# Optimization experiments

Hardware: AMD Instinct MI355X
Metric: run time of the kernel (lower is better)

Reference implementation:

```python
import jax, jax.numpy as jnp
import numpy as np

NUM_USERS = 100000
NUM_MOVIES = 50000
NUM_EDGES = 4000000
USER_FEAT = 24
MOVIE_FEAT = 404
HID = 64
GENRES = 3


def setup_inputs() -> dict:
    key = jax.random.key(0)
    ks = jax.random.split(key, 16)
    inp = {
        'x_user': jax.random.normal(ks[0], (NUM_USERS, USER_FEAT), jnp.float32),
        'x_movie': jax.random.normal(ks[1], (NUM_MOVIES, MOVIE_FEAT), jnp.float32),
        'edge_src': jax.random.randint(ks[2], (NUM_EDGES,), 0, NUM_USERS, jnp.int32),
        'edge_dst': jax.random.randint(ks[3], (NUM_EDGES,), 0, NUM_MOVIES, jnp.int32),
        'W_user': jax.random.normal(ks[4], (HID, USER_FEAT), jnp.float32) * 0.1,
        'b_user': jax.random.normal(ks[5], (HID,), jnp.float32) * 0.1,
        'W_movie': jax.random.normal(ks[6], (HID, MOVIE_FEAT), jnp.float32) * 0.05,
        'b_movie': jax.random.normal(ks[7], (HID,), jnp.float32) * 0.1,
        'Wl1_um': jax.random.normal(ks[8], (HID, HID), jnp.float32) * 0.1,
        'bl1_um': jax.random.normal(ks[9], (HID,), jnp.float32) * 0.1,
        'Wr1_um': jax.random.normal(ks[10], (HID, HID), jnp.float32) * 0.1,
        'Wl1_mu': jax.random.normal(ks[11], (HID, HID), jnp.float32) * 0.1,
        'bl1_mu': jax.random.normal(ks[12], (HID,), jnp.float32) * 0.1,
        'Wr1_mu': jax.random.normal(ks[13], (HID, HID), jnp.float32) * 0.1,
        'Wl2_um': jax.random.normal(ks[14], (GENRES, HID), jnp.float32) * 0.1,
        'bl2_um': jnp.zeros((GENRES,), jnp.float32),
        'Wr2_um': jax.random.normal(ks[15], (GENRES, HID), jnp.float32) * 0.1,
    }
    return inp


def _mean_agg(src_x, src_idx, dst_idx, num_dst):
    # gather messages [E, C], scatter-sum to dst, divide by degree (mean aggr)
    msg = src_x[src_idx]
    s = jax.ops.segment_sum(msg, dst_idx, num_segments=num_dst)
    cnt = jax.ops.segment_sum(jnp.ones_like(dst_idx, jnp.float32), dst_idx, num_segments=num_dst)
    return s / jnp.maximum(cnt, 1.0)[:, None]


def _sage(agg, x_dst, Wl, bl, Wr):
    # SAGEConv: lin_l(mean_aggr(x_j)) + lin_r(x_dst); bias only on lin_l
    return agg @ Wl.T + bl + x_dst @ Wr.T


def reference(x_user, x_movie, edge_src, edge_dst, W_user, b_user, W_movie, b_movie,
              Wl1_um, bl1_um, Wr1_um, Wl1_mu, bl1_mu, Wr1_mu, Wl2_um, bl2_um, Wr2_um):
    nu, nm = x_user.shape[0], x_movie.shape[0]
    # input projections
    hu = x_user @ W_user.T + b_user    # [U, H]
    hm = x_movie @ W_movie.T + b_movie  # [M, H]
    # layer 1 (hetero: one SAGEConv per edge type; undirected -> both directions)
    m1 = _sage(_mean_agg(hu, edge_src, edge_dst, nm), hm, Wl1_um, bl1_um, Wr1_um)
    u1 = _sage(_mean_agg(hm, edge_dst, edge_src, nu), hu, Wl1_mu, bl1_mu, Wr1_mu)
    m1 = jax.nn.relu(m1)
    u1 = jax.nn.relu(u1)
    # dropout is identity in eval mode
    # layer 2: only movie output is returned
    out = _sage(_mean_agg(u1, edge_src, edge_dst, nm), m1, Wl2_um, bl2_um, Wr2_um)
    return out
```

## Files before the change

kernel.cpp:

```cpp
#include <hip/hip_runtime.h>


constexpr int NU = 100000;
constexpr int NM = 50000;
constexpr int NE = 4000000;
constexpr int FU = 24;
constexpr int FM = 404;
constexpr int HD = 64;

constexpr int BSH = 8;
constexpr int MBK = (NM + 255) >> BSH;
constexpr int UBK = (NU + 255) >> BSH;
constexpr int NBK = MBK + UBK;
constexpr int EPB = 8192;
constexpr int CAPE = 28672;

static inline size_t alignup(size_t x) { return (x + 255) & ~size_t(255); }

__device__ __forceinline__ float bf2f(unsigned short h) {
  return __uint_as_float(((unsigned int)h) << 16);
}
__device__ __forceinline__ unsigned short f2bf(float f) {
  unsigned int u = __float_as_uint(f);
  u = (u + 0x7FFFu + ((u >> 16) & 1u)) >> 16;
  return (unsigned short)u;
}
__device__ __forceinline__ float2 unpk(unsigned u) {
  return make_float2(__uint_as_float(u << 16), __uint_as_float(u & 0xFFFF0000u));
}
__device__ __forceinline__ float fp8dec(unsigned v) {
  unsigned u = ((v & 0x80u) << 24) | ((v & 0x7Fu) << 20);
  return __uint_as_float(u) * 0x1p120f;
}
__device__ __forceinline__ unsigned char f2fp8(float f) {
  float a = fminf(fabsf(f), 448.0f);
  unsigned u = __float_as_uint(a * 0x1p-120f);
  u = u + 0x7FFFFu + ((u >> 20) & 1u);
  return (unsigned char)(((u >> 20) & 0x7Fu) | ((__float_as_uint(f) >> 24) & 0x80u));
}

typedef __attribute__((ext_vector_type(2))) float f2v;

#if __has_builtin(__builtin_amdgcn_cvt_pk_f32_fp8)
#define FP8_HW 1
#endif

__device__ __forceinline__ f2v fp8lo(unsigned w) {
#ifdef FP8_HW
  return __builtin_amdgcn_cvt_pk_f32_fp8(w, false);
#else
  f2v r; r.x = fp8dec(w); r.y = fp8dec(w >> 8); return r;
#endif
}
__device__ __forceinline__ f2v fp8hi(unsigned w) {
#ifdef FP8_HW
  return __builtin_amdgcn_cvt_pk_f32_fp8(w, true);
#else
  f2v r; r.x = fp8dec(w >> 16); r.y = fp8dec(w >> 24); return r;
#endif
}
__device__ __forceinline__ unsigned pk2bf(float x, float y) {
  return (unsigned)f2bf(x) | ((unsigned)f2bf(y) << 16);
}

using bf16x8 = __attribute__((ext_vector_type(8))) short;
using f32x4  = __attribute__((ext_vector_type(4))) float;


__global__ __launch_bounds__(256) void histB_kernel(const int* __restrict__ src,
                                                    const int* __restrict__ dst,
                                                    int* __restrict__ bh) {
  __shared__ int h[NBK];
  for (int i = threadIdx.x; i < NBK; i += 256) h[i] = 0;
  __syncthreads();
  int idx = blockIdx.x * 256 + threadIdx.x;
  int stride = gridDim.x * 256;
  for (int i = idx; i < NE; i += stride) {
    atomicAdd(&h[dst[i] >> BSH], 1);
    atomicAdd(&h[MBK + (src[i] >> BSH)], 1);
  }
  __syncthreads();
  for (int i = threadIdx.x; i < NBK; i += 256) {
    int c = h[i];
    if (c) atomicAdd(&bh[i], c);
  }
}

__global__ __launch_bounds__(1024) void scanB_kernel(const int* __restrict__ bh,
                                                     int* __restrict__ bbase_m,
                                                     int* __restrict__ bbase_u,
                                                     int* __restrict__ bcur_m,
                                                     int* __restrict__ bcur_u) {
  __shared__ int tmp[1024];
  int t = threadIdx.x;
  int vm = (t < MBK) ? bh[t] : 0;
  tmp[t] = vm;
  __syncthreads();
  for (int off = 1; off < 1024; off <<= 1) {
    int v = (t >= off) ? tmp[t - off] : 0;
    __syncthreads();
    tmp[t] += v;
    __syncthreads();
  }
  if (t < MBK) {
    int e = tmp[t] - vm;
    bbase_m[t] = e; bcur_m[t] = e;
    if (t == MBK - 1) bbase_m[MBK] = tmp[t];
  }
  __syncthreads();
  int vu = (t < UBK) ? bh[MBK + t] : 0;
  tmp[t] = vu;
  __syncthreads();
  for (int off = 1; off < 1024; off <<= 1) {
    int v = (t >= off) ? tmp[t - off] : 0;
    __syncthreads();
    tmp[t] += v;
    __syncthreads();
  }
  if (t < UBK) {
    int e = tmp[t] - vu;
    bbase_u[t] = e; bcur_u[t] = e;
    if (t == UBK - 1) bbase_u[UBK] = tmp[t];
  }
}

__global__ __launch_bounds__(1024) void passA_kernel(
    const int* __restrict__ src, const int* __restrict__ dst,
    int* __restrict__ bcur_m, int* __restrict__ bcur_u,
    unsigned* __restrict__ stage_m, unsigned* __restrict__ stage_u) {
  __shared__ int hB[NBK];
  __shared__ int cntB[NBK];
  __shared__ int gB[NBK];
  __shared__ int tmp[1024];
  __shared__ unsigned binM[EPB];
  __shared__ unsigned binU[EPB];
  int t = threadIdx.x;
  for (int i = t; i < NBK; i += 1024) hB[i] = 0;
  __syncthreads();
  int e0 = blockIdx.x * EPB + t;
  int sv[8], dv[8], rm[8], ru[8];
#pragma unroll
  for (int k = 0; k < 8; ++k) {
    int e = e0 + k * 1024;
    if (e < NE) {
      int s = src[e], d = dst[e];
      sv[k] = s; dv[k] = d;
      rm[k] = atomicAdd(&hB[d >> BSH], 1);
      ru[k] = atomicAdd(&hB[MBK + (s >> BSH)], 1);
    } else {
      sv[k] = -1;
    }
  }
  __syncthreads();
  int cm = (t < MBK) ? hB[t] : 0;
  tmp[t] = cm;
  __syncthreads();
  for (int off = 1; off < 1024; off <<= 1) {
    int v = (t >= off) ? tmp[t - off] : 0;
    __syncthreads();
    tmp[t] += v;
    __syncthreads();
  }
  int lofsM = tmp[t] - cm;
  __syncthreads();
  int cu_ = (t < UBK) ? hB[MBK + t] : 0;
  tmp[t] = cu_;
  __syncthreads();
  for (int off = 1; off < 1024; off <<= 1) {
    int v = (t >= off) ? tmp[t - off] : 0;
    __syncthreads();
    tmp[t] += v;
    __syncthreads();
  }
  int lofsU = tmp[t] - cu_;
  __syncthreads();
  if (t < MBK) { cntB[t] = cm; hB[t] = lofsM; }
  if (t < UBK) { cntB[MBK + t] = cu_; hB[MBK + t] = lofsU; }
  __syncthreads();
#pragma unroll
  for (int k = 0; k < 8; ++k) {
    if (sv[k] >= 0) {
      int s = sv[k], d = dv[k];
      binM[hB[d >> BSH] + rm[k]] = ((unsigned)(d & 255) << 24) | (unsigned)s;
      binU[hB[MBK + (s >> BSH)] + ru[k]] = ((unsigned)(s & 255) << 24) | (unsigned)d;
    }
  }
  __syncthreads();
  for (int b = t; b < NBK; b += 1024) {
    int cc = cntB[b];
    if (cc) {
      int gb = (b < MBK) ? atomicAdd(&bcur_m[b], cc) : atomicAdd(&bcur_u[b - MBK], cc);
      gB[b] = gb - hB[b];
    }
  }
  __syncthreads();
  int wv = t >> 6, ln = t & 63;
  for (int b = wv; b < MBK; b += 16) {
    int cc = cntB[b], lo = hB[b], go = hB[b] + gB[b];
    for (int j = ln; j < cc; j += 64) stage_m[go + j] = binM[lo + j];
  }
  for (int b = wv; b < UBK; b += 16) {
    int cc = cntB[MBK + b], lo = hB[MBK + b], go = hB[MBK + b] + gB[MBK + b];
    for (int j = ln; j < cc; j += 64) stage_u[go + j] = binU[lo + j];
  }
}

__global__ __launch_bounds__(1024) void passB_kernel(
    const int* __restrict__ bbase_m, const int* __restrict__ bbase_u,
    const unsigned* __restrict__ stage_m, const unsigned* __restrict__ stage_u,
    int* __restrict__ csr_m, int* __restrict__ csr_u,
    int* __restrict__ rp_m, int* __restrict__ rp_u) {
  __shared__ int cnt[256];
  __shared__ int sc[256];
  extern __shared__ unsigned sbuf[];
  int b = blockIdx.x;
  const unsigned* stage; int* csr; int* rp; int idbase, ntot, bb, be;
  if (b < MBK) {
    stage = stage_m; csr = csr_m; rp = rp_m;
    idbase = b << BSH; ntot = NM;
    bb = bbase_m[b]; be = bbase_m[b + 1];
  } else {
    int c = b - MBK;
    stage = stage_u; csr = csr_u; rp = rp_u;
    idbase = c << BSH; ntot = NU;
    bb = bbase_u[c]; be = bbase_u[c + 1];
  }
  int nloc = min(256, ntot - idbase);
  int t = threadIdx.x;
  int span = be - bb;
  if (t < 256) cnt[t] = 0;
  __syncthreads();
  for (int j = bb + t; j < be; j += 1024) atomicAdd(&cnt[stage[j] >> 24], 1);
  __syncthreads();
  int c0 = (t < 256) ? cnt[t] : 0;
  if (t < 256) sc[t] = c0;
  __syncthreads();
  for (int off = 1; off < 256; off <<= 1) {
    int v = 0;
    if (t < 256 && t >= off) v = sc[t - off];
    __syncthreads();
    if (t < 256) sc[t] += v;
    __syncthreads();
  }
  if (t < nloc) {
    rp[idbase + t] = bb + sc[t] - c0;
    cnt[t] = sc[t] - c0;
  }
  if (t == 0 && idbase + nloc == ntot) rp[ntot] = be;
  __syncthreads();
  if (span <= CAPE) {
    for (int j = bb + t; j < be; j += 1024) {
      unsigned e = stage[j];
      int pos = atomicAdd(&cnt[e >> 24], 1);
      sbuf[pos] = e & 0xFFFFFFu;
    }
    __syncthreads();
    for (int j = t; j < span; j += 1024) csr[bb + j] = (int)sbuf[j];
  } else {
    for (int j = bb + t; j < be; j += 1024) {
      unsigned e = stage[j];
      int pos = atomicAdd(&cnt[e >> 24], 1);
      csr[bb + pos] = (int)(e & 0xFFFFFFu);
    }
  }
}


__global__ void convXu_kernel(const float* __restrict__ xu, unsigned char* __restrict__ xu8) {
  int i = blockIdx.x * 256 + threadIdx.x;
  if (i < NU * 32) {
    int r = i >> 5, c = i & 31;
    xu8[i] = (c < FU) ? f2fp8(xu[r * FU + c]) : 0;
  }
}

__global__ void convXu16_kernel(const float* __restrict__ xu, unsigned short* __restrict__ xb) {
  int i = blockIdx.x * 256 + threadIdx.x;
  if (i < NU * 32) {
    int r = i >> 5, c = i & 31;
    unsigned short v = 0;
    if (c < FU) v = f2bf(xu[r * FU + c]);
    else if (c == 31) v = 0x3F80;
    xb[i] = v;
  }
}

__global__ void convW_kernel(const float* __restrict__ W, unsigned short* __restrict__ Wb,
                             int n) {
  int i = blockIdx.x * 256 + threadIdx.x;
  if (i < n) Wb[i] = f2bf(W[i]);
}

__global__ void convWum_kernel(const float* __restrict__ Wl, const float* __restrict__ Wu,
                               const float* __restrict__ bu, const float* __restrict__ Wr,
                               unsigned short* __restrict__ W96) {
  int i = blockIdx.x * 256 + threadIdx.x;
  if (i >= 64 * 96) return;
  int h = i / 96, k = i - h * 96;
  float v = 0.f;
  if (k < FU) {
    for (int j = 0; j < 64; ++j) v += Wl[h * 64 + j] * Wu[j * FU + k];
  } else if (k == 31) {
    for (int j = 0; j < 64; ++j) v += Wl[h * 64 + j] * bu[j];
  } else if (k >= 32) {
    v = Wr[h * 64 + (k - 32)];
  }
  W96[i] = f2bf(v);
}

__global__ void convWmu_kernel(const float* __restrict__ Wl, const float* __restrict__ Wr,
                               const float* __restrict__ Wu, const float* __restrict__ bu,
                               unsigned short* __restrict__ W96) {
  int i = blockIdx.x * 256 + threadIdx.x;
  if (i >= 64 * 96) return;
  int h = i / 96, k = i - h * 96;
  float v = 0.f;
  if (k < 64) {
    v = Wl[h * 64 + k];
  } else if (k < 64 + FU) {
    for (int j = 0; j < 64; ++j) v += Wr[h * 64 + j] * Wu[j * FU + (k - 64)];
  } else if (k == 95) {
    for (int j = 0; j < 64; ++j) v += Wr[h * 64 + j] * bu[j];
  }
  W96[i] = f2bf(v);
}

__global__ __launch_bounds__(256) void proj_movie_kernel(
    const float* __restrict__ xm, const unsigned short* __restrict__ Wb,
    const float* __restrict__ bm, unsigned short* __restrict__ hm,
    unsigned char* __restrict__ hm8) {
  __shared__ unsigned short Xs[64][72];
  __shared__ unsigned short Ws[64][72];
  int t = threadIdx.x;
  int lane = t & 63, wid = t >> 6;
  int row0 = blockIdx.x * 64;
  int r0 = wid * 16;
  f32x4 acc[4];
#pragma unroll
  for (int nt = 0; nt < 4; ++nt) acc[nt] = (f32x4){0.f, 0.f, 0.f, 0.f};

  for (int k0 = 0; k0 < 448; k0 += 64) {
    int kc = min(64, FM - k0);
    __syncthreads();
    for (int i = t; i < 1024; i += 256) {
      int r = i >> 4, c4 = i & 15;
      float4 v = make_float4(0.f, 0.f, 0.f, 0.f);
      if (c4 * 4 < kc && row0 + r < NM)
        v = *(const float4*)(xm + (size_t)(row0 + r) * FM + k0 + c4 * 4);
      ushort4 o;
      o.x = f2bf(v.x); o.y = f2bf(v.y); o.z = f2bf(v.z); o.w = f2bf(v.w);
      *(ushort4*)&Xs[r][c4 * 4] = o;
    }
    for (int i = t; i < 1024; i += 256) {
      int h = i >> 4, c4 = i & 15;
      uint2 v = make_uint2(0u, 0u);
      if (c4 * 4 < kc)
        v = *(const uint2*)(Wb + (size_t)h * FM + k0 + c4 * 4);
      *(uint2*)&Ws[h][c4 * 4] = v;
    }
    __syncthreads();
#pragma unroll
    for (int kk = 0; kk < 64; kk += 32) {
      bf16x8 a = *(const bf16x8*)&Xs[r0 + (lane & 15)][kk + (lane >> 4) * 8];
#pragma unroll
      for (int nt = 0; nt < 4; ++nt) {
        bf16x8 b = *(const bf16x8*)&Ws[nt * 16 + (lane & 15)][kk + (lane >> 4) * 8];
        acc[nt] = __builtin_amdgcn_mfma_f32_16x16x32_bf16(a, b, acc[nt], 0, 0, 0);
      }
    }
  }
  int col = lane & 15;
  int rbase = r0 + (lane >> 4) * 4;
#pragma unroll
  for (int nt = 0; nt < 4; ++nt) {
    float b = bm[nt * 16 + col];
#pragma unroll
    for (int j = 0; j < 4; ++j) {
      int row = row0 + rbase + j;
      if (row < NM) {
        float v = acc[nt][j] + b;
        hm[(size_t)row * HD + nt * 16 + col] = f2bf(v);
        hm8[(size_t)row * HD + nt * 16 + col] = f2fp8(v);
      }
    }
  }
}


__global__ __launch_bounds__(256) void agg24z_kernel(
    const unsigned char* __restrict__ xu8, const int* __restrict__ rp,
    const int* __restrict__ csr, unsigned short* __restrict__ a24,
    float* __restrict__ zagg, int n) {
  int wid = threadIdx.x >> 6, lane = threadIdx.x & 63;
  int g = lane >> 3, fq = lane & 7;
  int row = blockIdx.x * 32 + wid * 8 + g;
  if (row >= n) return;
  int beg = rp[row], end = rp[row + 1];
  const unsigned char* tb = xu8 + fq * 4;
  f2v a01 = {0.f, 0.f}, a23 = {0.f, 0.f};
  int i = beg;
  for (; i + 4 <= end; i += 4) {
    unsigned o0 = (unsigned)csr[i] << 5;
    unsigned o1 = (unsigned)csr[i + 1] << 5;
    unsigned o2 = (unsigned)csr[i + 2] << 5;
    unsigned o3 = (unsigned)csr[i + 3] << 5;
    unsigned w0 = *(const unsigned*)(tb + o0);
    unsigned w1 = *(const unsigned*)(tb + o1);
    unsigned w2 = *(const unsigned*)(tb + o2);
    unsigned w3 = *(const unsigned*)(tb + o3);
    a01 += (fp8lo(w0) + fp8lo(w1)) + (fp8lo(w2) + fp8lo(w3));
    a23 += (fp8hi(w0) + fp8hi(w1)) + (fp8hi(w2) + fp8hi(w3));
  }
  for (; i < end; ++i) {
    unsigned w = *(const unsigned*)(tb + ((unsigned)csr[i] << 5));
    a01 += fp8lo(w);
    a23 += fp8hi(w);
  }
  float inv = 1.0f / fmaxf((float)(end - beg), 1.0f);
  uint2 o;
  o.x = pk2bf(a01.x * inv, a01.y * inv);
  o.y = pk2bf(a23.x * inv, a23.y * inv);
  if (fq == 7)
    o.y = (o.y & 0xFFFFu) | ((end > beg ? 0x3F80u : 0u) << 16);
  if (fq == 6)
    *(float4*)(zagg + (size_t)row * 4) =
        make_float4(a01.x * inv, a01.y * inv, a23.x * inv, 0.f);
  *(uint2*)(a24 + (size_t)row * 32 + fq * 4) = o;
}


__global__ __launch_bounds__(256) void aggU_kernel(
    const unsigned char* __restrict__ tab8, const int* __restrict__ rp,
    const int* __restrict__ csr, unsigned short* __restrict__ out, int n) {
  int wid = threadIdx.x >> 6, lane = threadIdx.x & 63;
  int g = lane >> 3, fq = lane & 7;
  int row = blockIdx.x * 32 + wid * 8 + g;
  if (row >= n) return;
  int beg = rp[row], end = rp[row + 1];
  const unsigned char* tb = tab8 + fq * 8;
  f2v a01 = {0.f, 0.f}, a23 = {0.f, 0.f}, a45 = {0.f, 0.f}, a67 = {0.f, 0.f};
  int i = beg;
  for (; i + 4 <= end; i += 4) {
    unsigned o0 = (unsigned)csr[i] << 6;
    unsigned o1 = (unsigned)csr[i + 1] << 6;
    unsigned o2 = (unsigned)csr[i + 2] << 6;
    unsigned o3 = (unsigned)csr[i + 3] << 6;
    uint2 w0 = *(const uint2*)(tb + o0);
    uint2 w1 = *(const uint2*)(tb + o1);
    uint2 w2 = *(const uint2*)(tb + o2);
    uint2 w3 = *(const uint2*)(tb + o3);
    a01 += (fp8lo(w0.x) + fp8lo(w1.x)) + (fp8lo(w2.x) + fp8lo(w3.x));
    a23 += (fp8hi(w0.x) + fp8hi(w1.x)) + (fp8hi(w2.x) + fp8hi(w3.x));
    a45 += (fp8lo(w0.y) + fp8lo(w1.y)) + (fp8lo(w2.y) + fp8lo(w3.y));
    a67 += (fp8hi(w0.y) + fp8hi(w1.y)) + (fp8hi(w2.y) + fp8hi(w3.y));
  }
  for (; i < end; ++i) {
    uint2 w = *(const uint2*)(tb + ((unsigned)csr[i] << 6));
    a01 += fp8lo(w.x); a23 += fp8hi(w.x);
    a45 += fp8lo(w.y); a67 += fp8hi(w.y);
  }
  float inv = 1.0f / fmaxf((float)(end - beg), 1.0f);
  uint4 o;
  o.x = pk2bf(a01.x * inv, a01.y * inv);
  o.y = pk2bf(a23.x * inv, a23.y * inv);
  o.z = pk2bf(a45.x * inv, a45.y * inv);
  o.w = pk2bf(a67.x * inv, a67.y * inv);
  *(uint4*)(out + (size_t)row * HD + fq * 8) = o;
}


__global__ __launch_bounds__(256) void sage_um_kernel(
    const unsigned short* __restrict__ a24, const unsigned short* __restrict__ hm,
    const unsigned short* __restrict__ W96, const float* __restrict__ bl,
    unsigned short* __restrict__ m1, int n) {
  __shared__ unsigned short Xs[64][104];
  __shared__ unsigned short Ws[64][104];
  int t = threadIdx.x;
  int lane = t & 63, wid = t >> 6;
  int row0 = blockIdx.x * 64;
  int r0 = wid * 16;
  for (int i = t; i < 768; i += 256) {
    int h = i / 12, g = i - h * 12;
    *(uint4*)&Ws[h][g * 8] = *(const uint4*)(W96 + (size_t)h * 96 + g * 8);
  }
  for (int i = t; i < 768; i += 256) {
    int r = i / 12, g = i - r * 12;
    uint4 v = make_uint4(0u, 0u, 0u, 0u);
    if (row0 + r < n) {
      if (g < 4) v = *(const uint4*)(a24 + (size_t)(row0 + r) * 32 + g * 8);
      else       v = *(const uint4*)(hm + (size_t)(row0 + r) * HD + (g - 4) * 8);
    }
    *(uint4*)&Xs[r][g * 8] = v;
  }
  __syncthreads();
  f32x4 acc[4];
#pragma unroll
  for (int nt = 0; nt < 4; ++nt) acc[nt] = (f32x4){0.f, 0.f, 0.f, 0.f};
#pragma unroll
  for (int kk = 0; kk < 96; kk += 32) {
    bf16x8 a = *(const bf16x8*)&Xs[r0 + (lane & 15)][kk + (lane >> 4) * 8];
#pragma unroll
    for (int nt = 0; nt < 4; ++nt) {
      bf16x8 b = *(const bf16x8*)&Ws[nt * 16 + (lane & 15)][kk + (lane >> 4) * 8];
      acc[nt] = __builtin_amdgcn_mfma_f32_16x16x32_bf16(a, b, acc[nt], 0, 0, 0);
    }
  }
  int col = lane & 15;
  int rbase = r0 + (lane >> 4) * 4;
#pragma unroll
  for (int nt = 0; nt < 4; ++nt) {
    float b = bl[nt * 16 + col];
#pragma unroll
    for (int j = 0; j < 4; ++j) {
      int row = row0 + rbase + j;
      if (row < n)
        m1[(size_t)row * HD + nt * 16 + col] = f2bf(fmaxf(acc[nt][j] + b, 0.f));
    }
  }
}


__global__ __launch_bounds__(256) void sage96u_kernel(
    const unsigned short* __restrict__ agg, const unsigned short* __restrict__ xb,
    const unsigned short* __restrict__ W96, const float* __restrict__ bl,
    unsigned short* __restrict__ u1, int n) {
  __shared__ unsigned short Xs[64][104];
  __shared__ unsigned short Ws[64][104];
  int t = threadIdx.x;
  int lane = t & 63, wid = t >> 6;
  int row0 = blockIdx.x * 64;
  int r0 = wid * 16;
  for (int i = t; i < 768; i += 256) {
    int h = i / 12, g = i - h * 12;
    *(uint4*)&Ws[h][g * 8] = *(const uint4*)(W96 + (size_t)h * 96 + g * 8);
  }
  for (int i = t; i < 768; i += 256) {
    int r = i / 12, g = i - r * 12;
    uint4 v = make_uint4(0u, 0u, 0u, 0u);
    if (row0 + r < n) {
      if (g < 8) v = *(const uint4*)(agg + (size_t)(row0 + r) * HD + g * 8);
      else       v = *(const uint4*)(xb + (size_t)(row0 + r) * 32 + (g - 8) * 8);
    }
    *(uint4*)&Xs[r][g * 8] = v;
  }
  __syncthreads();
  f32x4 acc[4];
#pragma unroll
  for (int nt = 0; nt < 4; ++nt) acc[nt] = (f32x4){0.f, 0.f, 0.f, 0.f};
#pragma unroll
  for (int kk = 0; kk < 96; kk += 32) {
    bf16x8 a = *(const bf16x8*)&Xs[r0 + (lane & 15)][kk + (lane >> 4) * 8];
#pragma unroll
    for (int nt = 0; nt < 4; ++nt) {
      bf16x8 b = *(const bf16x8*)&Ws[nt * 16 + (lane & 15)][kk + (lane >> 4) * 8];
      acc[nt] = __builtin_amdgcn_mfma_f32_16x16x32_bf16(a, b, acc[nt], 0, 0, 0);
    }
  }
  int col = lane & 15;
  int rbase = r0 + (lane >> 4) * 4;
#pragma unroll
  for (int nt = 0; nt < 4; ++nt) {
    float b = bl[nt * 16 + col];
#pragma unroll
    for (int j = 0; j < 4; ++j) {
      int row = row0 + rbase + j;
      if (row < n)
        u1[(size_t)row * HD + nt * 16 + col] = f2bf(fmaxf(acc[nt][j] + b, 0.f));
    }
  }
}


__global__ __launch_bounds__(256) void zproj_kernel(
    const unsigned short* __restrict__ u1, const float* __restrict__ Wl2,
    unsigned char* __restrict__ xu8) {
  __shared__ float W[3][64];
  int t = threadIdx.x;
  if (t < 192) W[t / 64][t & 63] = Wl2[t];
  __syncthreads();
  int wid = t >> 6, lane = t & 63;
  int g = lane >> 4, fq = lane & 15;
  int row = blockIdx.x * 16 + wid * 4 + g;
  if (row >= NU) return;
  uint2 v = *(const uint2*)(u1 + (size_t)row * HD + fq * 4);
  float2 p0 = unpk(v.x), p1 = unpk(v.y);
  int f = fq * 4;
  float z0 = p0.x * W[0][f] + p0.y * W[0][f + 1] + p1.x * W[0][f + 2] + p1.y * W[0][f + 3];
  float z1 = p0.x * W[1][f] + p0.y * W[1][f + 1] + p1.x * W[1][f + 2] + p1.y * W[1][f + 3];
  float z2 = p0.x * W[2][f] + p0.y * W[2][f + 1] + p1.x * W[2][f + 2] + p1.y * W[2][f + 3];
#pragma unroll
  for (int off = 1; off < 16; off <<= 1) {
    z0 += __shfl_xor(z0, off);
    z1 += __shfl_xor(z1, off);
    z2 += __shfl_xor(z2, off);
  }
  if (fq == 0) {
    unsigned w = (unsigned)f2fp8(z0) | ((unsigned)f2fp8(z1) << 8)
               | ((unsigned)f2fp8(z2) << 16);
    *(unsigned*)(xu8 + (size_t)row * 32 + 24) = w;
  }
}

__global__ void out2_kernel(const float* __restrict__ zagg,
                            const unsigned short* __restrict__ m1,
                            const float* __restrict__ Wr2, const float* __restrict__ bl2,
                            float* __restrict__ out, int n) {
  int wid = threadIdx.x >> 6, lane = threadIdx.x & 63;
  int row = blockIdx.x * 4 + wid;
  if (row >= n) return;
  float mm = bf2f(m1[(size_t)row * HD + lane]);
#pragma unroll
  for (int g = 0; g < 3; ++g) {
    float p = mm * Wr2[g * HD + lane];
#pragma unroll
    for (int off = 32; off > 0; off >>= 1) p += __shfl_down(p, off);
    if (lane == 0) out[row * 3 + g] = p + zagg[row * 4 + g] + bl2[g];
  }
}


extern "C" void kernel_launch(void* const* d_in, const int* in_sizes, int n_in,
                              void* d_out, int out_size, void* d_ws, size_t ws_size,
                              hipStream_t stream) {
  const float* x_user  = (const float*)d_in[0];
  const float* x_movie = (const float*)d_in[1];
  const int*   e_src   = (const int*)d_in[2];
  const int*   e_dst   = (const int*)d_in[3];
  const float* W_user  = (const float*)d_in[4];
  const float* b_user  = (const float*)d_in[5];
  const float* W_movie = (const float*)d_in[6];
  const float* b_movie = (const float*)d_in[7];
  const float* Wl1_um  = (const float*)d_in[8];
  const float* bl1_um  = (const float*)d_in[9];
  const float* Wr1_um  = (const float*)d_in[10];
  const float* Wl1_mu  = (const float*)d_in[11];
  const float* bl1_mu  = (const float*)d_in[12];
  const float* Wr1_mu  = (const float*)d_in[13];
  const float* Wl2_um  = (const float*)d_in[14];
  const float* bl2_um  = (const float*)d_in[15];
  const float* Wr2_um  = (const float*)d_in[16];
  float* outp = (float*)d_out;

  char* p = (char*)d_ws;
  size_t off = 0;
  auto take = [&](size_t bytes) { void* r = p + off; off += alignup(bytes); return r; };

  int* rp_m    = (int*)take(size_t(NM + 1) * 4);
  int* rp_u    = (int*)take(size_t(NU + 1) * 4);
  int* bh      = (int*)take(size_t(NBK) * 4);
  int* bbase_m = (int*)take(size_t(MBK + 1) * 4);
  int* bbase_u = (int*)take(size_t(UBK + 1) * 4);
  int* bcur_m  = (int*)take(size_t(MBK) * 4);
  int* bcur_u  = (int*)take(size_t(UBK) * 4);
  int* csr_m   = (int*)take(size_t(NE) * 4);
  int* csr_u   = (int*)take(size_t(NE) * 4);

  size_t ov_base = off;
  unsigned* stage_m = (unsigned*)take(size_t(NE) * 4);
  unsigned* stage_u = (unsigned*)take(size_t(NE) * 4);
  size_t stage_end = off;
  off = ov_base;
  unsigned short* hm    = (unsigned short*)take(size_t(NM) * HD * 2);
  unsigned short* u1    = (unsigned short*)take(size_t(NU) * HD * 2);
  unsigned short* m1    = (unsigned short*)take(size_t(NM) * HD * 2);
  unsigned short* aggb  = (unsigned short*)take(size_t(NU) * HD * 2);
  unsigned char*  xu8   = (unsigned char*)take(size_t(NU) * 32);
  unsigned char*  hm8   = (unsigned char*)take(size_t(NM) * HD);
  unsigned short* a24   = (unsigned short*)take(size_t(NM) * 32 * 2);
  unsigned short* xub16 = (unsigned short*)take(size_t(NU) * 32 * 2);
  if (off < stage_end) off = stage_end;
  float* zagg = (float*)take(size_t(NM) * 16);
  unsigned short* Wb    = (unsigned short*)take(size_t(HD) * FM * 2);
  unsigned short* Wum96 = (unsigned short*)take(size_t(HD) * 96 * 2);
  unsigned short* Wmu96 = (unsigned short*)take(size_t(HD) * 96 * 2);
  if (off > ws_size) return;

  const int TB = 256;

  hipMemsetAsync(bh, 0, size_t(NBK) * 4, stream);
  histB_kernel<<<512, 256, 0, stream>>>(e_src, e_dst, bh);
  scanB_kernel<<<1, 1024, 0, stream>>>(bh, bbase_m, bbase_u, bcur_m, bcur_u);
  passA_kernel<<<(NE + EPB - 1) / EPB, 1024, 0, stream>>>(e_src, e_dst, bcur_m, bcur_u,
                                                          stage_m, stage_u);
  passB_kernel<<<NBK, 1024, CAPE * 4, stream>>>(bbase_m, bbase_u, stage_m, stage_u,
                                                csr_m, csr_u, rp_m, rp_u);

  convW_kernel<<<(HD * FM + 255) / 256, 256, 0, stream>>>(W_movie, Wb, HD * FM);
  convWum_kernel<<<(64 * 96 + 255) / 256, 256, 0, stream>>>(Wl1_um, W_user, b_user,
                                                            Wr1_um, Wum96);
  convWmu_kernel<<<(64 * 96 + 255) / 256, 256, 0, stream>>>(Wl1_mu, Wr1_mu, W_user,
                                                            b_user, Wmu96);
  convXu_kernel<<<(NU * 32 + 255) / 256, 256, 0, stream>>>(x_user, xu8);
  convXu16_kernel<<<(NU * 32 + 255) / 256, 256, 0, stream>>>(x_user, xub16);
  proj_movie_kernel<<<(NM + 63) / 64, TB, 0, stream>>>(x_movie, Wb, b_movie, hm, hm8);

  aggU_kernel<<<(NU + 31) / 32, TB, 0, stream>>>(hm8, rp_u, csr_u, aggb, NU);
  sage96u_kernel<<<(NU + 63) / 64, TB, 0, stream>>>(aggb, xub16, Wmu96, bl1_mu, u1, NU);
  zproj_kernel<<<(NU + 15) / 16, TB, 0, stream>>>(u1, Wl2_um, xu8);

  agg24z_kernel<<<(NM + 31) / 32, TB, 0, stream>>>(xu8, rp_m, csr_m, a24, zagg, NM);
  sage_um_kernel<<<(NM + 63) / 64, TB, 0, stream>>>(a24, hm, Wum96, bl1_um, m1, NM);

  out2_kernel<<<(NM + 3) / 4, TB, 0, stream>>>(zagg, m1, Wr2_um, bl2_um, outp, NM);
}
```

Before: 270.1 us.

## Preload padded movie weights to LDS and double-buffer X tiles in projection

The movie weight matrix is padded to 448 columns and loaded into shared memory once per block, instead of being re-staged each k-chunk. The x_movie tile is double-buffered: the next chunk's global loads are issued into registers before the MFMA work on the current chunk and written to the other LDS buffer afterwards, leaving one barrier per iteration. This aims to hide global-load latency in proj_movie, which streams about 80MB of fp32 input. In exchange, LDS use rises to about 77KB per block, which may lower occupancy, and more registers are held live.

```diff
diff --git a/kernel.cpp b/kernel.cpp
--- a/kernel.cpp
+++ b/kernel.cpp
@@ -285,10 +285,12 @@
   }
 }
 
-__global__ void convW_kernel(const float* __restrict__ W, unsigned short* __restrict__ Wb,
-                             int n) {
+__global__ void convW_kernel(const float* __restrict__ W, unsigned short* __restrict__ Wb) {
   int i = blockIdx.x * 256 + threadIdx.x;
-  if (i < n) Wb[i] = f2bf(W[i]);
+  if (i < HD * 448) {
+    int h = i / 448, k = i - h * 448;
+    Wb[i] = (k < FM) ? f2bf(W[h * FM + k]) : 0;
+  }
 }
 
 __global__ void convWum_kernel(const float* __restrict__ Wl, const float* __restrict__ Wu,
@@ -329,46 +331,65 @@
     const float* __restrict__ xm, const unsigned short* __restrict__ Wb,
     const float* __restrict__ bm, unsigned short* __restrict__ hm,
     unsigned char* __restrict__ hm8) {
-  __shared__ unsigned short Xs[64][72];
-  __shared__ unsigned short Ws[64][72];
+  __shared__ unsigned short Ws[64][456];
+  __shared__ unsigned short Xs[2][64][72];
   int t = threadIdx.x;
   int lane = t & 63, wid = t >> 6;
   int row0 = blockIdx.x * 64;
   int r0 = wid * 16;
-  f32x4 acc[4];
-#pragma unroll
-  for (int nt = 0; nt < 4; ++nt) acc[nt] = (f32x4){0.f, 0.f, 0.f, 0.f};
-
-  for (int k0 = 0; k0 < 448; k0 += 64) {
-    int kc = min(64, FM - k0);
-    __syncthreads();
-    for (int i = t; i < 1024; i += 256) {
+
+  for (int i = t; i < 3584; i += 256) {
+    int h = i / 56, g = i - h * 56;
+    *(uint4*)&Ws[h][g * 8] = *(const uint4*)(Wb + (size_t)h * 448 + g * 8);
+  }
+
+  float4 xr[4];
+  auto loadX = [&](int k0) {
+#pragma unroll
+    for (int j = 0; j < 4; ++j) {
+      int i = t + j * 256;
       int r = i >> 4, c4 = i & 15;
       float4 v = make_float4(0.f, 0.f, 0.f, 0.f);
-      if (c4 * 4 < kc && row0 + r < NM)
+      if (k0 + c4 * 4 < FM && row0 + r < NM)
         v = *(const float4*)(xm + (size_t)(row0 + r) * FM + k0 + c4 * 4);
+      xr[j] = v;
+    }
+  };
+  auto writeX = [&](int buf) {
+#pragma unroll
+    for (int j = 0; j < 4; ++j) {
+      int i = t + j * 256;
+      int r = i >> 4, c4 = i & 15;
       ushort4 o;
-      o.x = f2bf(v.x); o.y = f2bf(v.y); o.z = f2bf(v.z); o.w = f2bf(v.w);
-      *(ushort4*)&Xs[r][c4 * 4] = o;
-    }
-    for (int i = t; i < 1024; i += 256) {
-      int h = i >> 4, c4 = i & 15;
-      uint2 v = make_uint2(0u, 0u);
-      if (c4 * 4 < kc)
-        v = *(const uint2*)(Wb + (size_t)h * FM + k0 + c4 * 4);
-      *(uint2*)&Ws[h][c4 * 4] = v;
-    }
-    __syncthreads();
+      o.x = f2bf(xr[j].x); o.y = f2bf(xr[j].y);
+      o.z = f2bf(xr[j].z); o.w = f2bf(xr[j].w);
+      *(ushort4*)&Xs[buf][r][c4 * 4] = o;
+    }
+  };
+
+  loadX(0);
+  writeX(0);
+  f32x4 acc[4];
+#pragma unroll
+  for (int nt = 0; nt < 4; ++nt) acc[nt] = (f32x4){0.f, 0.f, 0.f, 0.f};
+
+  for (int c = 0; c < 7; ++c) {
+    if (c < 6) loadX((c + 1) * 64);
+    __syncthreads();
+    int buf = c & 1;
+    int kbase = c * 64;
 #pragma unroll
     for (int kk = 0; kk < 64; kk += 32) {
-      bf16x8 a = *(const bf16x8*)&Xs[r0 + (lane & 15)][kk + (lane >> 4) * 8];
+      bf16x8 a = *(const bf16x8*)&Xs[buf][r0 + (lane & 15)][kk + (lane >> 4) * 8];
 #pragma unroll
       for (int nt = 0; nt < 4; ++nt) {
-        bf16x8 b = *(const bf16x8*)&Ws[nt * 16 + (lane & 15)][kk + (lane >> 4) * 8];
+        bf16x8 b = *(const bf16x8*)&Ws[nt * 16 + (lane & 15)][kbase + kk + (lane >> 4) * 8];
         acc[nt] = __builtin_amdgcn_mfma_f32_16x16x32_bf16(a, b, acc[nt], 0, 0, 0);
       }
     }
-  }
+    if (c < 6) writeX((c + 1) & 1);
+  }
+
   int col = lane & 15;
   int rbase = r0 + (lane >> 4) * 4;
 #pragma unroll
@@ -670,7 +691,7 @@
   unsigned short* xub16 = (unsigned short*)take(size_t(NU) * 32 * 2);
   if (off < stage_end) off = stage_end;
   float* zagg = (float*)take(size_t(NM) * 16);
-  unsigned short* Wb    = (unsigned short*)take(size_t(HD) * FM * 2);
+  unsigned short* Wb    = (unsigned short*)take(size_t(HD) * 448 * 2);
   unsigned short* Wum96 = (unsigned short*)take(size_t(HD) * 96 * 2);
   unsigned short* Wmu96 = (unsigned short*)take(size_t(HD) * 96 * 2);
   if (off > ws_size) return;
@@ -685,7 +706,7 @@
   passB_kernel<<<NBK, 1024, CAPE * 4, stream>>>(bbase_m, bbase_u, stage_m, stage_u,
                                                 csr_m, csr_u, rp_m, rp_u);
 
-  convW_kernel<<<(HD * FM + 255) / 256, 256, 0, stream>>>(W_movie, Wb, HD * FM);
+  convW_kernel<<<(HD * 448 + 255) / 256, 256, 0, stream>>>(W_movie, Wb);
   convWum_kernel<<<(64 * 96 + 255) / 256, 256, 0, stream>>>(Wl1_um, W_user, b_user,
                                                             Wr1_um, Wum96);
   convWmu_kernel<<<(64 * 96 + 255) / 256, 256, 0, stream>>>(Wl1_mu, Wr1_mu, W_user,
```

Result: no change. 270.6 us (+0.2%).
